# Kernel tuning notes

Measured on AMD Instinct MI355X. Metric: run time of the kernel, lower is better.

Reference implementation:

```python
import jax, jax.numpy as jnp
import numpy as np

N = 2_000_000
CLAMP_THR = 0.9999999


def quat_to_rot(q):
    # q: [N,4] (unnormalized) -> [N,3,3] rotation matrices
    q = q / jnp.linalg.norm(q, axis=-1, keepdims=True)
    w, x, y, z = q[:, 0], q[:, 1], q[:, 2], q[:, 3]
    R = jnp.stack([
        jnp.stack([1 - 2 * (y * y + z * z), 2 * (x * y - w * z), 2 * (x * z + w * y)], axis=-1),
        jnp.stack([2 * (x * y + w * z), 1 - 2 * (x * x + z * z), 2 * (y * z - w * x)], axis=-1),
        jnp.stack([2 * (x * z - w * y), 2 * (y * z + w * x), 1 - 2 * (x * x + y * y)], axis=-1),
    ], axis=-2)
    return R


def setup_inputs() -> dict:
    key = jax.random.key(0)
    k1, k2, k3 = jax.random.split(key, 3)
    R_w2c1 = quat_to_rot(jax.random.normal(k1, (N, 4), dtype=jnp.float32))
    R_w2c2 = quat_to_rot(jax.random.normal(k2, (N, 4), dtype=jnp.float32))
    # small-angle noise rotation so residuals are realistic (cos inside clamp)
    q_noise = jnp.concatenate(
        [jnp.ones((N, 1), dtype=jnp.float32), 0.05 * jax.random.normal(k3, (N, 3), dtype=jnp.float32)],
        axis=-1)
    Rn = quat_to_rot(q_noise)
    # R_rel ~= R_w2c2 @ R_w2c1^T composed with noise
    R_rel = jnp.einsum('nij,njk->nik', jnp.einsum('nij,nkj->nik', R_w2c2, R_w2c1), Rn)
    return {"R_rel": R_rel, "R_w2c1": R_w2c1, "R_w2c2": R_w2c2}


def reference(R_rel, R_w2c1, R_w2c2):
    # residual M = R_rel^T @ R_w2c2 @ R_w2c1^T should be identity;
    # cos(theta) = (tr(M) - 1) / 2
    tr = jnp.einsum('nji,njk,nik->n', R_rel, R_w2c2, R_w2c1)
    cos = 0.5 * (tr - 1.0)
    cos_c = jnp.clip(cos, -CLAMP_THR, CLAMP_THR)
    loss = jnp.sum(jnp.arccos(cos_c))[None]  # shape (1,), matching the CUDA buffer
    # analytic gradient of sum arccos(cos) wrt R_w2c1, R_w2c2;
    # zero where the clamp is active (derivative of clip is 0 there)
    g = jnp.where(jnp.abs(cos) < CLAMP_THR,
                  -0.5 / jnp.sqrt(1.0 - cos_c * cos_c),
                  jnp.zeros_like(cos))  # includes d cos / d tr = 0.5
    # d tr / d R_w2c1 = R_rel^T @ R_w2c2 ; d tr / d R_w2c2 = R_rel @ R_w2c1
    d_R_w2c1 = g[:, None, None] * jnp.einsum('nji,njk->nik', R_rel, R_w2c2)
    d_R_w2c2 = g[:, None, None] * jnp.einsum('nij,njk->nik', R_rel, R_w2c1)
    return loss, d_R_w2c1, d_R_w2c2
```

## Files before the change

### kernel.cpp

```cpp
#include <hip/hip_runtime.h>

#define CLAMP_THR 0.9999999f

typedef float f4a __attribute__((ext_vector_type(4), aligned(4)));

__global__ void zero_loss_kernel(float* out) {
    if (threadIdx.x == 0) out[0] = 0.0f;
}

template<bool USE_WS>
__global__ __launch_bounds__(256) void geodesic_direct_kernel(
    const float* __restrict__ Rrel,
    const float* __restrict__ Rw1,
    const float* __restrict__ Rw2,
    float* __restrict__ out,
    float* __restrict__ ws,
    int n)
{
    __shared__ float wsum[4];
    const int t = threadIdx.x;
    const int e = blockIdx.x * 256 + t;

    float local_loss = 0.0f;
    if (e < n) {
        const size_t b = (size_t)e * 9;
        float R[9], A[9], B[9];

        f4a v;
        v = *(const f4a*)(Rrel + b);     R[0]=v.x; R[1]=v.y; R[2]=v.z; R[3]=v.w;
        v = *(const f4a*)(Rrel + b + 4); R[4]=v.x; R[5]=v.y; R[6]=v.z; R[7]=v.w;
        R[8] = Rrel[b + 8];
        v = *(const f4a*)(Rw2 + b);      A[0]=v.x; A[1]=v.y; A[2]=v.z; A[3]=v.w;
        v = *(const f4a*)(Rw2 + b + 4);  A[4]=v.x; A[5]=v.y; A[6]=v.z; A[7]=v.w;
        A[8] = Rw2[b + 8];
        v = *(const f4a*)(Rw1 + b);      B[0]=v.x; B[1]=v.y; B[2]=v.z; B[3]=v.w;
        v = *(const f4a*)(Rw1 + b + 4);  B[4]=v.x; B[5]=v.y; B[6]=v.z; B[7]=v.w;
        B[8] = Rw1[b + 8];

        float M[9];
        #pragma unroll
        for (int i = 0; i < 3; ++i)
            #pragma unroll
            for (int k = 0; k < 3; ++k)
                M[3 * i + k] = R[i]     * A[k]
                             + R[3 + i] * A[3 + k]
                             + R[6 + i] * A[6 + k];
        float tr = 0.0f;
        #pragma unroll
        for (int j = 0; j < 9; ++j) tr += M[j] * B[j];

        float cosv = 0.5f * (tr - 1.0f);
        float cosc = fminf(fmaxf(cosv, -CLAMP_THR), CLAMP_THR);
        local_loss = acosf(cosc);
        float g = (fabsf(cosv) < CLAMP_THR)
                    ? (-0.5f / sqrtf(1.0f - cosc * cosc))
                    : 0.0f;

        float* __restrict__ o1 = out + 1 + b;
        f4a s;
        s.x = g*M[0]; s.y = g*M[1]; s.z = g*M[2]; s.w = g*M[3];
        *(f4a*)(o1) = s;
        s.x = g*M[4]; s.y = g*M[5]; s.z = g*M[6]; s.w = g*M[7];
        *(f4a*)(o1 + 4) = s;
        o1[8] = g*M[8];

        float D[9];
        #pragma unroll
        for (int i = 0; i < 3; ++i)
            #pragma unroll
            for (int k = 0; k < 3; ++k)
                D[3 * i + k] = g * (R[3 * i]     * B[k]
                                  + R[3 * i + 1] * B[3 + k]
                                  + R[3 * i + 2] * B[6 + k]);
        float* __restrict__ o2 = out + 1 + (size_t)n * 9 + b;
        s.x = D[0]; s.y = D[1]; s.z = D[2]; s.w = D[3];
        *(f4a*)(o2) = s;
        s.x = D[4]; s.y = D[5]; s.z = D[6]; s.w = D[7];
        *(f4a*)(o2 + 4) = s;
        o2[8] = D[8];
    }

    #pragma unroll
    for (int off = 32; off > 0; off >>= 1)
        local_loss += __shfl_down(local_loss, off, 64);
    if ((t & 63) == 0) wsum[t >> 6] = local_loss;
    __syncthreads();
    if (t == 0) {
        const float blocksum = wsum[0] + wsum[1] + wsum[2] + wsum[3];
        if (USE_WS) ws[blockIdx.x] = blocksum;
        else        atomicAdd(out, blocksum);
    }
}

__global__ __launch_bounds__(1024) void reduce_loss_kernel(
    const float* __restrict__ ws, int nb, float* __restrict__ out)
{
    __shared__ float wsum[16];
    const int t = threadIdx.x;
    float s = 0.0f;
    for (int i = t; i < nb; i += 1024) s += ws[i];
    #pragma unroll
    for (int off = 32; off > 0; off >>= 1)
        s += __shfl_down(s, off, 64);
    if ((t & 63) == 0) wsum[t >> 6] = s;
    __syncthreads();
    if (t == 0) {
        float tot = 0.0f;
        #pragma unroll
        for (int i = 0; i < 16; ++i) tot += wsum[i];
        out[0] = tot;
    }
}

extern "C" void kernel_launch(void* const* d_in, const int* in_sizes, int n_in,
                              void* d_out, int out_size, void* d_ws, size_t ws_size,
                              hipStream_t stream) {
    const float* Rrel = (const float*)d_in[0];
    const float* Rw1  = (const float*)d_in[1];
    const float* Rw2  = (const float*)d_in[2];
    float* out = (float*)d_out;
    const int n = in_sizes[0] / 9;
    const int nb = (n + 255) / 256;

    if (ws_size >= (size_t)nb * sizeof(float)) {
        geodesic_direct_kernel<true><<<nb, 256, 0, stream>>>(
            Rrel, Rw1, Rw2, out, (float*)d_ws, n);
        reduce_loss_kernel<<<1, 1024, 0, stream>>>((const float*)d_ws, nb, out);
    } else {
        zero_loss_kernel<<<1, 64, 0, stream>>>(out);
        geodesic_direct_kernel<false><<<nb, 256, 0, stream>>>(
            Rrel, Rw1, Rw2, out, nullptr, n);
    }
}
```

Before: 299.3 us.

## Transpose gradient outputs through LDS for coalesced stores and per-wave loss partials

Each wave stages its 64x9 gradient values in shared memory and writes them back as contiguous, lane-strided scalar stores instead of per-thread strided vector stores. The output at offset out+1 is misaligned for 16-byte accesses, so this makes the stores fully coalesced. The block-level reduction and __syncthreads are replaced by per-wave partial sums written to the workspace, which quadruples the number of partials the final reduce kernel reads. Inputs are still loaded with per-thread strided vector loads. The LDS round trip adds latency and wave-local fences.

```diff
diff --git a/kernel.cpp b/kernel.cpp
--- a/kernel.cpp
+++ b/kernel.cpp
@@ -8,8 +8,14 @@
     if (threadIdx.x == 0) out[0] = 0.0f;
 }
 
+__device__ __forceinline__ void lds_fence() {
+    __builtin_amdgcn_wave_barrier();
+    asm volatile("s_waitcnt lgkmcnt(0)" ::: "memory");
+    __builtin_amdgcn_wave_barrier();
+}
+
 template<bool USE_WS>
-__global__ __launch_bounds__(256) void geodesic_direct_kernel(
+__global__ __launch_bounds__(256) void geodesic_tp_kernel(
     const float* __restrict__ Rrel,
     const float* __restrict__ Rw1,
     const float* __restrict__ Rw2,
@@ -17,11 +23,18 @@
     float* __restrict__ ws,
     int n)
 {
-    __shared__ float wsum[4];
-    const int t = threadIdx.x;
-    const int e = blockIdx.x * 256 + t;
+    __shared__ float tp[4][576];
+
+    const int t    = threadIdx.x;
+    const int lane = t & 63;
+    const int w    = t >> 6;
+    const int e    = blockIdx.x * 256 + t;
+    const int wbase = blockIdx.x * 256 + w * 64;
+    const bool full = (wbase + 64 <= n);
 
     float local_loss = 0.0f;
+    float D1[9], D2[9];
+
     if (e < n) {
         const size_t b = (size_t)e * 9;
         float R[9], A[9], B[9];
@@ -56,49 +69,63 @@
                     ? (-0.5f / sqrtf(1.0f - cosc * cosc))
                     : 0.0f;
 
-        float* __restrict__ o1 = out + 1 + b;
-        f4a s;
-        s.x = g*M[0]; s.y = g*M[1]; s.z = g*M[2]; s.w = g*M[3];
-        *(f4a*)(o1) = s;
-        s.x = g*M[4]; s.y = g*M[5]; s.z = g*M[6]; s.w = g*M[7];
-        *(f4a*)(o1 + 4) = s;
-        o1[8] = g*M[8];
-
-        float D[9];
+        #pragma unroll
+        for (int j = 0; j < 9; ++j) D1[j] = g * M[j];
         #pragma unroll
         for (int i = 0; i < 3; ++i)
             #pragma unroll
             for (int k = 0; k < 3; ++k)
-                D[3 * i + k] = g * (R[3 * i]     * B[k]
-                                  + R[3 * i + 1] * B[3 + k]
-                                  + R[3 * i + 2] * B[6 + k]);
-        float* __restrict__ o2 = out + 1 + (size_t)n * 9 + b;
-        s.x = D[0]; s.y = D[1]; s.z = D[2]; s.w = D[3];
-        *(f4a*)(o2) = s;
-        s.x = D[4]; s.y = D[5]; s.z = D[6]; s.w = D[7];
-        *(f4a*)(o2 + 4) = s;
-        o2[8] = D[8];
+                D2[3 * i + k] = g * (R[3 * i]     * B[k]
+                                   + R[3 * i + 1] * B[3 + k]
+                                   + R[3 * i + 2] * B[6 + k]);
+    }
+
+    float* __restrict__ out1 = out + 1;
+    float* __restrict__ out2 = out + 1 + (size_t)n * 9;
+
+    if (full) {
+        float* buf = tp[w];
+        const size_t wb9 = (size_t)wbase * 9;
+
+        #pragma unroll
+        for (int c = 0; c < 9; ++c) buf[9 * lane + c] = D1[c];
+        lds_fence();
+        #pragma unroll
+        for (int j = 0; j < 9; ++j)
+            out1[wb9 + 64 * j + lane] = buf[64 * j + lane];
+        lds_fence();
+
+        #pragma unroll
+        for (int c = 0; c < 9; ++c) buf[9 * lane + c] = D2[c];
+        lds_fence();
+        #pragma unroll
+        for (int j = 0; j < 9; ++j)
+            out2[wb9 + 64 * j + lane] = buf[64 * j + lane];
+    } else if (e < n) {
+        const size_t b = (size_t)e * 9;
+        #pragma unroll
+        for (int j = 0; j < 9; ++j) out1[b + j] = D1[j];
+        #pragma unroll
+        for (int j = 0; j < 9; ++j) out2[b + j] = D2[j];
     }
 
     #pragma unroll
     for (int off = 32; off > 0; off >>= 1)
         local_loss += __shfl_down(local_loss, off, 64);
-    if ((t & 63) == 0) wsum[t >> 6] = local_loss;
-    __syncthreads();
-    if (t == 0) {
-        const float blocksum = wsum[0] + wsum[1] + wsum[2] + wsum[3];
-        if (USE_WS) ws[blockIdx.x] = blocksum;
-        else        atomicAdd(out, blocksum);
+    if (lane == 0) {
+        const int gw = blockIdx.x * 4 + w;
+        if (USE_WS) ws[gw] = local_loss;
+        else if (local_loss != 0.0f) atomicAdd(out, local_loss);
     }
 }
 
 __global__ __launch_bounds__(1024) void reduce_loss_kernel(
-    const float* __restrict__ ws, int nb, float* __restrict__ out)
+    const float* __restrict__ ws, int nw, float* __restrict__ out)
 {
     __shared__ float wsum[16];
     const int t = threadIdx.x;
     float s = 0.0f;
-    for (int i = t; i < nb; i += 1024) s += ws[i];
+    for (int i = t; i < nw; i += 1024) s += ws[i];
     #pragma unroll
     for (int off = 32; off > 0; off >>= 1)
         s += __shfl_down(s, off, 64);
@@ -119,16 +146,17 @@
     const float* Rw1  = (const float*)d_in[1];
     const float* Rw2  = (const float*)d_in[2];
     float* out = (float*)d_out;
-    const int n = in_sizes[0] / 9;
+    const int n  = in_sizes[0] / 9;
     const int nb = (n + 255) / 256;
+    const int nw = nb * 4;
 
-    if (ws_size >= (size_t)nb * sizeof(float)) {
-        geodesic_direct_kernel<true><<<nb, 256, 0, stream>>>(
+    if (ws_size >= (size_t)nw * sizeof(float)) {
+        geodesic_tp_kernel<true><<<nb, 256, 0, stream>>>(
             Rrel, Rw1, Rw2, out, (float*)d_ws, n);
-        reduce_loss_kernel<<<1, 1024, 0, stream>>>((const float*)d_ws, nb, out);
+        reduce_loss_kernel<<<1, 1024, 0, stream>>>((const float*)d_ws, nw, out);
     } else {
         zero_loss_kernel<<<1, 64, 0, stream>>>(out);
-        geodesic_direct_kernel<false><<<nb, 256, 0, stream>>>(
+        geodesic_tp_kernel<false><<<nb, 256, 0, stream>>>(
             Rrel, Rw1, Rw2, out, nullptr, n);
     }
 }
```

After: 307.0 us. 2.6% more time.

## Use grid-stride loop with register prefetch and nontemporal stores

Applied to the files above, without the earlier changes.

Replaces the one-element-per-thread launch with a grid capped at 2048 blocks and a grid-stride loop. Each thread loads the next element's 27 floats while it computes and stores the current one, and the outputs are written with nontemporal stores. The aim is to overlap load latency with compute, reduce block launch overhead and the size of the partial-sum reduction, and keep streaming outputs from polluting the cache. It doubles the input registers per thread, which could lower occupancy, and a persistent grid may hide latency less well than many blocks in flight.

```diff
diff --git a/kernel.cpp b/kernel.cpp
--- a/kernel.cpp
+++ b/kernel.cpp
@@ -8,8 +8,72 @@
     if (threadIdx.x == 0) out[0] = 0.0f;
 }
 
+__device__ __forceinline__ void load27(const float* __restrict__ Rrel,
+                                       const float* __restrict__ Rw2,
+                                       const float* __restrict__ Rw1,
+                                       size_t b,
+                                       float R[9], float A[9], float B[9])
+{
+    f4a v;
+    v = *(const f4a*)(Rrel + b);     R[0]=v.x; R[1]=v.y; R[2]=v.z; R[3]=v.w;
+    v = *(const f4a*)(Rrel + b + 4); R[4]=v.x; R[5]=v.y; R[6]=v.z; R[7]=v.w;
+    R[8] = Rrel[b + 8];
+    v = *(const f4a*)(Rw2 + b);      A[0]=v.x; A[1]=v.y; A[2]=v.z; A[3]=v.w;
+    v = *(const f4a*)(Rw2 + b + 4);  A[4]=v.x; A[5]=v.y; A[6]=v.z; A[7]=v.w;
+    A[8] = Rw2[b + 8];
+    v = *(const f4a*)(Rw1 + b);      B[0]=v.x; B[1]=v.y; B[2]=v.z; B[3]=v.w;
+    v = *(const f4a*)(Rw1 + b + 4);  B[4]=v.x; B[5]=v.y; B[6]=v.z; B[7]=v.w;
+    B[8] = Rw1[b + 8];
+}
+
+__device__ __forceinline__ float compute_store(
+    const float R[9], const float A[9], const float B[9],
+    float* __restrict__ o1, float* __restrict__ o2)
+{
+    float M[9];
+    #pragma unroll
+    for (int i = 0; i < 3; ++i)
+        #pragma unroll
+        for (int k = 0; k < 3; ++k)
+            M[3 * i + k] = R[i]     * A[k]
+                         + R[3 + i] * A[3 + k]
+                         + R[6 + i] * A[6 + k];
+    float tr = 0.0f;
+    #pragma unroll
+    for (int j = 0; j < 9; ++j) tr += M[j] * B[j];
+
+    const float cosv = 0.5f * (tr - 1.0f);
+    const float cosc = fminf(fmaxf(cosv, -CLAMP_THR), CLAMP_THR);
+    const float g = (fabsf(cosv) < CLAMP_THR)
+                      ? (-0.5f / sqrtf(1.0f - cosc * cosc))
+                      : 0.0f;
+
+    f4a s;
+    s.x = g*M[0]; s.y = g*M[1]; s.z = g*M[2]; s.w = g*M[3];
+    __builtin_nontemporal_store(s, (f4a*)o1);
+    s.x = g*M[4]; s.y = g*M[5]; s.z = g*M[6]; s.w = g*M[7];
+    __builtin_nontemporal_store(s, (f4a*)(o1 + 4));
+    __builtin_nontemporal_store(g*M[8], o1 + 8);
+
+    float D[9];
+    #pragma unroll
+    for (int i = 0; i < 3; ++i)
+        #pragma unroll
+        for (int k = 0; k < 3; ++k)
+            D[3 * i + k] = g * (R[3 * i]     * B[k]
+                              + R[3 * i + 1] * B[3 + k]
+                              + R[3 * i + 2] * B[6 + k]);
+    s.x = D[0]; s.y = D[1]; s.z = D[2]; s.w = D[3];
+    __builtin_nontemporal_store(s, (f4a*)o2);
+    s.x = D[4]; s.y = D[5]; s.z = D[6]; s.w = D[7];
+    __builtin_nontemporal_store(s, (f4a*)(o2 + 4));
+    __builtin_nontemporal_store(D[8], o2 + 8);
+
+    return acosf(cosc);
+}
+
 template<bool USE_WS>
-__global__ __launch_bounds__(256) void geodesic_direct_kernel(
+__global__ __launch_bounds__(256) void geodesic_gs_kernel(
     const float* __restrict__ Rrel,
     const float* __restrict__ Rw1,
     const float* __restrict__ Rw2,
@@ -19,65 +83,28 @@
 {
     __shared__ float wsum[4];
     const int t = threadIdx.x;
-    const int e = blockIdx.x * 256 + t;
+    const int stride = gridDim.x * 256;
+    int e = blockIdx.x * 256 + t;
+
+    float* __restrict__ out1 = out + 1;
+    float* __restrict__ out2 = out + 1 + (size_t)n * 9;
 
     float local_loss = 0.0f;
-    if (e < n) {
+    float R[9], A[9], B[9];
+    float Rn[9], An[9], Bn[9];
+
+    if (e < n) load27(Rrel, Rw2, Rw1, (size_t)e * 9, R, A, B);
+
+    for (; e < n; e += stride) {
+        const int en = e + stride;
+        if (en < n)
+            load27(Rrel, Rw2, Rw1, (size_t)en * 9, Rn, An, Bn);
+
         const size_t b = (size_t)e * 9;
-        float R[9], A[9], B[9];
+        local_loss += compute_store(R, A, B, out1 + b, out2 + b);
 
-        f4a v;
-        v = *(const f4a*)(Rrel + b);     R[0]=v.x; R[1]=v.y; R[2]=v.z; R[3]=v.w;
-        v = *(const f4a*)(Rrel + b + 4); R[4]=v.x; R[5]=v.y; R[6]=v.z; R[7]=v.w;
-        R[8] = Rrel[b + 8];
-        v = *(const f4a*)(Rw2 + b);      A[0]=v.x; A[1]=v.y; A[2]=v.z; A[3]=v.w;
-        v = *(const f4a*)(Rw2 + b + 4);  A[4]=v.x; A[5]=v.y; A[6]=v.z; A[7]=v.w;
-        A[8] = Rw2[b + 8];
-        v = *(const f4a*)(Rw1 + b);      B[0]=v.x; B[1]=v.y; B[2]=v.z; B[3]=v.w;
-        v = *(const f4a*)(Rw1 + b + 4);  B[4]=v.x; B[5]=v.y; B[6]=v.z; B[7]=v.w;
-        B[8] = Rw1[b + 8];
-
-        float M[9];
         #pragma unroll
-        for (int i = 0; i < 3; ++i)
-            #pragma unroll
-            for (int k = 0; k < 3; ++k)
-                M[3 * i + k] = R[i]     * A[k]
-                             + R[3 + i] * A[3 + k]
-                             + R[6 + i] * A[6 + k];
-        float tr = 0.0f;
-        #pragma unroll
-        for (int j = 0; j < 9; ++j) tr += M[j] * B[j];
-
-        float cosv = 0.5f * (tr - 1.0f);
-        float cosc = fminf(fmaxf(cosv, -CLAMP_THR), CLAMP_THR);
-        local_loss = acosf(cosc);
-        float g = (fabsf(cosv) < CLAMP_THR)
-                    ? (-0.5f / sqrtf(1.0f - cosc * cosc))
-                    : 0.0f;
-
-        float* __restrict__ o1 = out + 1 + b;
-        f4a s;
-        s.x = g*M[0]; s.y = g*M[1]; s.z = g*M[2]; s.w = g*M[3];
-        *(f4a*)(o1) = s;
-        s.x = g*M[4]; s.y = g*M[5]; s.z = g*M[6]; s.w = g*M[7];
-        *(f4a*)(o1 + 4) = s;
-        o1[8] = g*M[8];
-
-        float D[9];
-        #pragma unroll
-        for (int i = 0; i < 3; ++i)
-            #pragma unroll
-            for (int k = 0; k < 3; ++k)
-                D[3 * i + k] = g * (R[3 * i]     * B[k]
-                                  + R[3 * i + 1] * B[3 + k]
-                                  + R[3 * i + 2] * B[6 + k]);
-        float* __restrict__ o2 = out + 1 + (size_t)n * 9 + b;
-        s.x = D[0]; s.y = D[1]; s.z = D[2]; s.w = D[3];
-        *(f4a*)(o2) = s;
-        s.x = D[4]; s.y = D[5]; s.z = D[6]; s.w = D[7];
-        *(f4a*)(o2 + 4) = s;
-        o2[8] = D[8];
+        for (int j = 0; j < 9; ++j) { R[j] = Rn[j]; A[j] = An[j]; B[j] = Bn[j]; }
     }
 
     #pragma unroll
@@ -92,24 +119,19 @@
     }
 }
 
-__global__ __launch_bounds__(1024) void reduce_loss_kernel(
+__global__ __launch_bounds__(256) void reduce_loss_kernel(
     const float* __restrict__ ws, int nb, float* __restrict__ out)
 {
-    __shared__ float wsum[16];
+    __shared__ float wsum[4];
     const int t = threadIdx.x;
     float s = 0.0f;
-    for (int i = t; i < nb; i += 1024) s += ws[i];
+    for (int i = t; i < nb; i += 256) s += ws[i];
     #pragma unroll
     for (int off = 32; off > 0; off >>= 1)
         s += __shfl_down(s, off, 64);
     if ((t & 63) == 0) wsum[t >> 6] = s;
     __syncthreads();
-    if (t == 0) {
-        float tot = 0.0f;
-        #pragma unroll
-        for (int i = 0; i < 16; ++i) tot += wsum[i];
-        out[0] = tot;
-    }
+    if (t == 0) out[0] = wsum[0] + wsum[1] + wsum[2] + wsum[3];
 }
 
 extern "C" void kernel_launch(void* const* d_in, const int* in_sizes, int n_in,
@@ -120,15 +142,17 @@
     const float* Rw2  = (const float*)d_in[2];
     float* out = (float*)d_out;
     const int n = in_sizes[0] / 9;
-    const int nb = (n + 255) / 256;
 
-    if (ws_size >= (size_t)nb * sizeof(float)) {
-        geodesic_direct_kernel<true><<<nb, 256, 0, stream>>>(
+    const int nChunks = (n + 255) / 256;
+    const int grid = nChunks < 2048 ? nChunks : 2048;
+
+    if (ws_size >= (size_t)grid * sizeof(float)) {
+        geodesic_gs_kernel<true><<<grid, 256, 0, stream>>>(
             Rrel, Rw1, Rw2, out, (float*)d_ws, n);
-        reduce_loss_kernel<<<1, 1024, 0, stream>>>((const float*)d_ws, nb, out);
+        reduce_loss_kernel<<<1, 256, 0, stream>>>((const float*)d_ws, grid, out);
     } else {
         zero_loss_kernel<<<1, 64, 0, stream>>>(out);
-        geodesic_direct_kernel<false><<<nb, 256, 0, stream>>>(
+        geodesic_gs_kernel<false><<<grid, 256, 0, stream>>>(
             Rrel, Rw1, Rw2, out, nullptr, n);
     }
 }
```

After: 365.3 us. 22.1% more time.
